# Kernel tuning notes

Hardware: AMD Instinct MI355X
Metric: run time of the kernel (lower is better)

The kernel has to match this reference:

```python
import jax, jax.numpy as jnp
import numpy as np

B, T, N, M = 64, 128, 128, 512


def setup_inputs() -> dict:
    key = jax.random.key(0)
    ks = jax.random.split(key, 9)
    w = 0.02
    return dict(
        X=jax.random.normal(ks[0], (B, T, N), jnp.float32),
        h0=jax.random.normal(ks[1], (B, M), jnp.float32) * 0.05,
        s0=jax.random.normal(ks[2], (B, M), jnp.float32) * 0.05,
        # LSTM cell params (keras gate order: i, f, c, o)
        W_lstm=jax.random.normal(ks[3], (N, 4 * M), jnp.float32) * w,
        U_lstm=jax.random.normal(ks[4], (M, 4 * M), jnp.float32) * w,
        b_lstm=jnp.zeros((4 * M,), jnp.float32),
        # InputAttention params: W_e: Dense(T) on concat([h,c]) (2m -> T),
        # U_e: Dense(T) on X^T (T -> T), v_e: Dense(1) (T -> 1)
        W_e=jax.random.normal(ks[5], (2 * M, T), jnp.float32) * w,
        b_We=jnp.zeros((T,), jnp.float32),
        U_e=jax.random.normal(ks[6], (T, T), jnp.float32) * w,
        b_Ue=jnp.zeros((T,), jnp.float32),
        v_e=jax.random.normal(ks[7], (T, 1), jnp.float32) * w,
        b_ve=jnp.zeros((1,), jnp.float32),
    )


def reference(X, h0, s0, W_lstm, U_lstm, b_lstm, W_e, b_We, U_e, b_Ue, v_e, b_ve):
    # In the original, every loop iteration t runs a single LSTM step on
    # X[:, t, :] starting from the SAME initial_state [h0, s0] (state is not
    # carried across t), so all T steps are independent -> vectorize over T.
    z = jnp.einsum('btn,nk->btk', X, W_lstm) + (h0 @ U_lstm + b_lstm)[:, None, :]
    zi, zf, zc, zo = jnp.split(z, 4, axis=-1)  # keras gate order i,f,c,o
    i = jax.nn.sigmoid(zi)
    f = jax.nn.sigmoid(zf)
    o = jax.nn.sigmoid(zo)
    c = f * s0[:, None, :] + i * jnp.tanh(zc)  # (B, T, m)
    h = o * jnp.tanh(c)                        # (B, T, m)

    # InputAttention for every t at once:
    # e_t = v_e(tanh(W_e([h_t; c_t]) broadcast over n  +  U_e(X^T)))
    hc = jnp.concatenate([h, c], axis=-1)              # (B, T, 2m)
    A = hc @ W_e + b_We                                # (B, T, T)
    U = jnp.einsum('btn,tk->bnk', X, U_e) + b_Ue       # (B, n, T)
    e = jnp.tanh(A[:, :, None, :] + U[:, None, :, :])  # (B, T, n, T)
    scores = jnp.einsum('btnk,k->btn', e, v_e[:, 0]) + b_ve[0]  # (B, T, n)
    alpha = jax.nn.softmax(scores, axis=-1)            # softmax over n
    return X * alpha
```

## Files before the change

kernel.cpp:

```cpp
#include <hip/hip_runtime.h>

typedef __attribute__((ext_vector_type(8))) short bfrag;
typedef __attribute__((ext_vector_type(4))) float f32x4;

#define C_SCALE 2.885390081777926815f

__device__ __forceinline__ float fast_rcp(float x){
#if __has_builtin(__builtin_amdgcn_rcpf)
  return __builtin_amdgcn_rcpf(x);
#else
  return 1.0f/x;
#endif
}
__device__ __forceinline__ float fexp2(float x){
#if __has_builtin(__builtin_amdgcn_exp2f)
  return __builtin_amdgcn_exp2f(x);
#else
  return exp2f(x);
#endif
}
__device__ __forceinline__ float sigm(float x){ return fast_rcp(1.0f + __expf(-x)); }
__device__ __forceinline__ float tanh_f(float x){ return 1.0f - 2.0f*fast_rcp(__expf(2.0f*x) + 1.0f); }
__device__ __forceinline__ unsigned short f2bf(float f){
  unsigned u = __float_as_uint(f);
  return (unsigned short)((u + 0x7fffu + ((u>>16)&1u)) >> 16);
}
__device__ __forceinline__ void gload16(const void* g, void* l){
  __builtin_amdgcn_global_load_lds((const __attribute__((address_space(1))) void*)g,
                                   (__attribute__((address_space(3))) void*)l, 16, 0, 0);
}

__global__ __launch_bounds__(256) void prep(const float* __restrict__ X,
                                            unsigned short* __restrict__ Xbf,
                                            const float* __restrict__ Wl,
                                            unsigned short* __restrict__ Wlt,
                                            const float* __restrict__ We,
                                            unsigned short* __restrict__ Wet,
                                            const float* __restrict__ h0,
                                            const float* __restrict__ Ul,
                                            float* __restrict__ Uhp,
                                            const float* __restrict__ Ue,
                                            const float* __restrict__ bUe,
                                            unsigned short* __restrict__ UTb){
  __shared__ __align__(16) float sh[6600];
  const int tid = threadIdx.x;
  const int bid = blockIdx.x;

  if (bid < 512){
    const int i = (bid*256 + tid)*8;
    float4 a = *(const float4*)&X[i];
    float4 b = *(const float4*)&X[i+4];
    ushort4 lo, hi;
    lo.x=f2bf(a.x); lo.y=f2bf(a.y); lo.z=f2bf(a.z); lo.w=f2bf(a.w);
    hi.x=f2bf(b.x); hi.y=f2bf(b.y); hi.z=f2bf(b.z); hi.w=f2bf(b.w);
    *(ushort4*)&Xbf[i] = lo; *(ushort4*)&Xbf[i+4] = hi;
  } else if (bid < 608){
    const float* in; unsigned short* outp; int K, N, j0, k0, perm;
    if (bid < 576){ int r = bid-512; in = Wl; outp = Wlt; K = 128;  N = 2048; j0 = (r&31)*64; k0 = (r>>5)*64; perm = 0; }
    else          { int r = bid-576; in = We; outp = Wet; K = 1024; N = 128;  j0 = (r&1)*64;  k0 = (r>>1)*64; perm = 1; }
    float (*t)[68] = (float(*)[68])sh;
#pragma unroll
    for (int i=0;i<4;i++){
      int idx = tid + i*256;
      int r = idx>>4, c4 = idx&15;
      int kk = k0 + r;
      int srow = perm ? ((kk&1) ? 512 + (kk>>1) : (kk>>1)) : kk;
      *(float4*)&t[r][c4*4] = *(const float4*)&in[srow*N + j0 + c4*4];
    }
    __syncthreads();
#pragma unroll
    for (int i=0;i<4;i++){
      int idx = tid + i*256;
      int r = idx>>4, c4 = idx&15;
      ushort4 o;
      o.x = f2bf(t[c4*4+0][r]); o.y = f2bf(t[c4*4+1][r]);
      o.z = f2bf(t[c4*4+2][r]); o.w = f2bf(t[c4*4+3][r]);
      *(ushort4*)&outp[(j0+r)*K + k0 + c4*4] = o;
    }
  } else if (bid < 736){
    const int r = bid - 608;
    const int nh = r & 1, b = r >> 1;
    float (*Xs)[68]  = (float(*)[68])sh;
    float (*Us)[132] = (float(*)[132])(sh + 2176);
    const int tc5 = tid & 31, tr8 = tid >> 5;
    f32x4 a4[8];
#pragma unroll
    for (int j=0;j<8;j++) a4[j] = (f32x4){0.f,0.f,0.f,0.f};
    for (int tk=0; tk<4; tk++){
#pragma unroll
      for (int i=0;i<2;i++){
        int idx = tid + i*256;
        int t = idx>>4, nq = idx&15;
        *(float4*)&Xs[t][nq*4] = *(const float4*)&X[(b*128 + tk*32 + t)*128 + nh*64 + nq*4];
      }
#pragma unroll
      for (int i=0;i<4;i++){
        int idx = tid + i*256;
        int t = idx>>5, kq = idx&31;
        *(float4*)&Us[t][kq*4] = *(const float4*)&Ue[(tk*32+t)*128 + kq*4];
      }
      __syncthreads();
#pragma unroll 4
      for (int t=0;t<32;t++){
        f32x4 u4 = *(const f32x4*)&Us[t][tc5*4];
        f32x4 x0 = *(const f32x4*)&Xs[t][tr8*8];
        f32x4 x1 = *(const f32x4*)&Xs[t][tr8*8+4];
        a4[0] += x0.x*u4; a4[1] += x0.y*u4; a4[2] += x0.z*u4; a4[3] += x0.w*u4;
        a4[4] += x1.x*u4; a4[5] += x1.y*u4; a4[6] += x1.z*u4; a4[7] += x1.w*u4;
      }
      __syncthreads();
    }
    const f32x4 bu = *(const f32x4*)&bUe[tc5*4];
    const int ktile = tc5 >> 1, khalf = tc5 & 1;
#pragma unroll
    for (int j=0;j<8;j++){
      const int n = nh*64 + tr8*8 + j;
      f32x4 v = a4[j] + bu;
      ushort4 o;
      o.x = f2bf(fexp2(C_SCALE*v.x)); o.y = f2bf(fexp2(C_SCALE*v.y));
      o.z = f2bf(fexp2(C_SCALE*v.z)); o.w = f2bf(fexp2(C_SCALE*v.w));
      *(ushort4*)&UTb[b*16384 + ktile*1024 + n*8 + khalf*4] = o;
    }
  } else {
    const int r = bid - 736;
    const int jc = r & 15;
    const int bc = (r>>4) >> 2, kc = (r>>4) & 3;
    float (*h0s)[128] = (float(*)[128])sh;
#pragma unroll
    for (int i=0;i<2;i++){
      int idx = tid + i*256;
      int bi = idx>>5, kq = idx&31;
      *(float4*)&h0s[bi][kq*4] = *(const float4*)&h0[(bc*16+bi)*512 + kc*128 + kq*4];
    }
    __syncthreads();
    const int jj = tid & 127, bh = tid >> 7;
    const int j = jc*128 + jj;
    float acc[8];
#pragma unroll
    for (int i=0;i<8;i++) acc[i]=0.f;
    for (int k=0;k<128;k+=4){
      float w0 = Ul[(kc*128+k+0)*2048 + j];
      float w1 = Ul[(kc*128+k+1)*2048 + j];
      float w2 = Ul[(kc*128+k+2)*2048 + j];
      float w3 = Ul[(kc*128+k+3)*2048 + j];
#pragma unroll
      for (int bi=0;bi<8;bi++){
        float4 h4 = *(const float4*)&h0s[bh*8+bi][k];
        acc[bi] += h4.x*w0 + h4.y*w1 + h4.z*w2 + h4.w*w3;
      }
    }
#pragma unroll
    for (int bi=0;bi<8;bi++)
      Uhp[kc*131072 + (bc*16 + bh*8 + bi)*2048 + j] = acc[bi];
  }
}

__global__ __launch_bounds__(256) void k2_k(const unsigned short* __restrict__ Xbf,
                                            const unsigned short* __restrict__ Wlt,
                                            const float* __restrict__ Uhp,
                                            const float* __restrict__ bl,
                                            const float* __restrict__ s0,
                                            unsigned int* __restrict__ hci){
  __shared__ __align__(16) char lds[32768];
  const int tid = threadIdx.x;
  const int mc = blockIdx.x & 15, b = blockIdx.x >> 4;
  const int bt0 = b*128;
  const int lane = tid & 63, wave = tid >> 6;
  const int wr = wave >> 1, wc = wave & 1;

  f32x4 acc[4][4];
#pragma unroll
  for (int mt=0;mt<4;mt++)
#pragma unroll
    for (int nt=0;nt<4;nt++) acc[mt][nt] = (f32x4){0.f,0.f,0.f,0.f};

  for (int kh=0; kh<2; kh++){
#pragma unroll
    for (int i=0;i<4;i++){
      int g = tid + i*256;
      int r = g>>3, G = g&7;
      gload16(Xbf + (bt0+r)*128 + kh*64 + ((G ^ (r&7))<<3), lds + g*16);
    }
#pragma unroll
    for (int i=0;i<4;i++){
      int g = tid + i*256;
      int c = g>>3, G = g&7;
      int q = c>>4;
      int j = (q&3)*512 + mc*32 + ((q>>2)<<4) + (c&15);
      gload16(Wlt + j*128 + kh*64 + ((G ^ (c&7))<<3), lds + 16384 + g*16);
    }
    __syncthreads();
#pragma unroll
    for (int ks2=0; ks2<2; ks2++){
      const int kb = ks2*64 + ((lane>>4)<<4);
      bfrag a[4], bb[4];
#pragma unroll
      for (int mt=0;mt<4;mt++){
        int r = wr*64 + mt*16 + (lane&15);
        a[mt] = *(const bfrag*)&lds[r*128 + (kb ^ ((r&7)<<4))];
      }
#pragma unroll
      for (int nt=0;nt<4;nt++){
        int c = wc*64 + nt*16 + (lane&15);
        bb[nt] = *(const bfrag*)&lds[16384 + c*128 + (kb ^ ((c&7)<<4))];
      }
#pragma unroll
      for (int mt=0;mt<4;mt++)
#pragma unroll
        for (int nt=0;nt<4;nt++)
          acc[mt][nt] = __builtin_amdgcn_mfma_f32_16x16x32_bf16(a[mt], bb[nt], acc[mt][nt], 0, 0, 0);
    }
    __syncthreads();
  }

  const int mloc = mc*32 + wc*16 + (lane&15);
  float uh[4];
#pragma unroll
  for (int g=0;g<4;g++){
    int j = g*512 + mloc;
    uh[g] = bl[j] + Uhp[0*131072 + b*2048 + j] + Uhp[1*131072 + b*2048 + j]
                  + Uhp[2*131072 + b*2048 + j] + Uhp[3*131072 + b*2048 + j];
  }
  const float s0v = s0[b*512 + mloc];
#pragma unroll
  for (int mt=0;mt<4;mt++){
#pragma unroll
    for (int reg=0;reg<4;reg++){
      int row = wr*64 + mt*16 + (lane>>4)*4 + reg;
      float zi = acc[mt][0][reg] + uh[0];
      float zf = acc[mt][1][reg] + uh[1];
      float zc = acc[mt][2][reg] + uh[2];
      float zo = acc[mt][3][reg] + uh[3];
      float fi = sigm(zi), ff = sigm(zf), fo = sigm(zo);
      float cv = ff*s0v + fi*tanh_f(zc);
      float hv = fo*tanh_f(cv);
      hci[(bt0+row)*512 + mloc] = (unsigned)f2bf(hv) | ((unsigned)f2bf(cv) << 16);
    }
  }
}

__global__ __launch_bounds__(256) void k3_k(const unsigned short* __restrict__ hc,
                                            const unsigned short* __restrict__ Wet,
                                            const float* __restrict__ bWe,
                                            float* __restrict__ eA){
  __shared__ __align__(16) char lds[24576];
  const int nc = blockIdx.x & 1, rc = blockIdx.x >> 1;
  const int bt0 = rc*32;
  const int tid = threadIdx.x;
  const int lane = tid & 63, wave = tid >> 6;
  const int wr = wave >> 1, wc = wave & 1;

  f32x4 acc[2];
  acc[0] = (f32x4){0.f,0.f,0.f,0.f};
  acc[1] = (f32x4){0.f,0.f,0.f,0.f};

  for (int ks=0; ks<8; ks++){
    const int k0 = ks*128;
#pragma unroll
    for (int i=0;i<2;i++){
      int g = tid + i*256;
      int r = g>>4, G = g&15;
      gload16(hc + (bt0+r)*1024 + k0 + ((G ^ (r&7))<<3), lds + g*16);
    }
#pragma unroll
    for (int i=0;i<4;i++){
      int g = tid + i*256;
      int r = g>>4, G = g&15;
      gload16(Wet + (nc*64 + r)*1024 + k0 + ((G ^ (r&7))<<3), lds + 8192 + g*16);
    }
    __syncthreads();
#pragma unroll
    for (int kk=0;kk<4;kk++){
      const int kb = kk*64 + ((lane>>4)<<4);
      int r = wr*16 + (lane&15);
      bfrag a = *(const bfrag*)&lds[r*256 + (kb ^ ((r&7)<<4))];
      bfrag bb0, bb1;
      {
        int nn = wc*32 + 0*16 + (lane&15);
        bb0 = *(const bfrag*)&lds[8192 + nn*256 + (kb ^ ((nn&7)<<4))];
        nn = wc*32 + 1*16 + (lane&15);
        bb1 = *(const bfrag*)&lds[8192 + nn*256 + (kb ^ ((nn&7)<<4))];
      }
      acc[0] = __builtin_amdgcn_mfma_f32_16x16x32_bf16(a, bb0, acc[0], 0, 0, 0);
      acc[1] = __builtin_amdgcn_mfma_f32_16x16x32_bf16(a, bb1, acc[1], 0, 0, 0);
    }
    __syncthreads();
  }
#pragma unroll
  for (int reg=0; reg<4; reg++){
    int row = bt0 + wr*16 + (lane>>4)*4 + reg;
#pragma unroll
    for (int nt=0;nt<2;nt++){
      int col = nc*64 + wc*32 + nt*16 + (lane&15);
      eA[row*128 + col] = fexp2(C_SCALE*(acc[nt][reg] + bWe[col]));
    }
  }
}

__global__ __launch_bounds__(256) void k5_k(const float* __restrict__ X,
                                            const unsigned short* __restrict__ UTb,
                                            const float* __restrict__ eA,
                                            const float* __restrict__ ve,
                                            float* __restrict__ out){
  __shared__ __align__(16) float As[8*128];
  __shared__ __align__(16) float vs[128];
  __shared__ float redm[4][4], reds[4][4];
  const int tid = threadIdx.x;
  const int tch = blockIdx.x;
  const int b   = blockIdx.y;
  const int tpair = tid>>7, n = tid&127, wid = tid>>6;

  {
    const float* asrc = eA + (b*128 + tch*8)*128;
    gload16(asrc + tid*4, (char*)As + tid*16);
    if (tid < 128) vs[tid] = ve[tid];
  }
  __syncthreads();

  f32x4 sc[4];
#pragma unroll
  for (int tt=0;tt<4;tt++) sc[tt] = (f32x4){0.f,0.f,0.f,0.f};

  const unsigned short* urow = UTb + b*16384 + n*8;
#pragma unroll 4
  for (int k8=0; k8<16; k8++){
    uint4 u = *(const uint4*)(urow + k8*1024);
    f32x4 ua, ub;
    ua.x = __uint_as_float(u.x<<16); ua.y = __uint_as_float(u.x & 0xffff0000u);
    ua.z = __uint_as_float(u.y<<16); ua.w = __uint_as_float(u.y & 0xffff0000u);
    ub.x = __uint_as_float(u.z<<16); ub.y = __uint_as_float(u.z & 0xffff0000u);
    ub.z = __uint_as_float(u.w<<16); ub.w = __uint_as_float(u.w & 0xffff0000u);
    const f32x4 va = *(const f32x4*)&vs[k8*8];
    const f32x4 vb = *(const f32x4*)&vs[k8*8+4];
#pragma unroll
    for (int tt=0; tt<4; tt++){
      const float* Ar = &As[(tt*2+tpair)*128 + k8*8];
      f32x4 ea = *(const f32x4*)Ar;
      f32x4 eb = *(const f32x4*)(Ar+4);
      f32x4 ra, rb;
      ra.x = fast_rcp(ea.x*ua.x + 1.f); ra.y = fast_rcp(ea.y*ua.y + 1.f);
      ra.z = fast_rcp(ea.z*ua.z + 1.f); ra.w = fast_rcp(ea.w*ua.w + 1.f);
      rb.x = fast_rcp(eb.x*ub.x + 1.f); rb.y = fast_rcp(eb.y*ub.y + 1.f);
      rb.z = fast_rcp(eb.z*ub.z + 1.f); rb.w = fast_rcp(eb.w*ub.w + 1.f);
      sc[tt] += va*ra;
      sc[tt] += vb*rb;
    }
  }

  float sv[4];
#pragma unroll
  for (int tt=0;tt<4;tt++){
    float s = -2.f*((sc[tt].x + sc[tt].y) + (sc[tt].z + sc[tt].w));
    sv[tt] = s;
    float m = s;
#pragma unroll
    for (int off=32; off>0; off>>=1) m = fmaxf(m, __shfl_xor(m, off));
    if ((tid&63)==0) redm[wid][tt] = m;
  }
  __syncthreads();
  float evv[4];
#pragma unroll
  for (int tt=0;tt<4;tt++){
    const float M = fmaxf(redm[tpair*2][tt], redm[tpair*2+1][tt]);
    float e = __expf(sv[tt] - M);
    evv[tt] = e;
    float s = e;
#pragma unroll
    for (int off=32; off>0; off>>=1) s += __shfl_xor(s, off);
    if ((tid&63)==0) reds[wid][tt] = s;
  }
  __syncthreads();
#pragma unroll
  for (int tt=0;tt<4;tt++){
    const float S = reds[tpair*2][tt] + reds[tpair*2+1][tt];
    const float alpha = evv[tt] * fast_rcp(S);
    const int t = tch*8 + tt*2 + tpair;
    const int g = (b*128 + t)*128 + n;
    out[g] = X[g] * alpha;
  }
}

extern "C" void kernel_launch(void* const* d_in, const int* in_sizes, int n_in,
                              void* d_out, int out_size, void* d_ws, size_t ws_size,
                              hipStream_t stream){
  (void)in_sizes; (void)n_in; (void)out_size; (void)ws_size;
  const float* X   = (const float*)d_in[0];
  const float* h0  = (const float*)d_in[1];
  const float* s0  = (const float*)d_in[2];
  const float* Wl  = (const float*)d_in[3];
  const float* Ul  = (const float*)d_in[4];
  const float* bl  = (const float*)d_in[5];
  const float* We  = (const float*)d_in[6];
  const float* bWe = (const float*)d_in[7];
  const float* Ue  = (const float*)d_in[8];
  const float* bUe = (const float*)d_in[9];
  const float* ve  = (const float*)d_in[10];
  float* out = (float*)d_out;

  char* ws = (char*)d_ws;
  unsigned short* Wlt = (unsigned short*)(ws + 0);
  unsigned short* Wet = (unsigned short*)(ws + 524288);
  unsigned short* Xbf = (unsigned short*)(ws + 786432);
  unsigned short* UTb = (unsigned short*)(ws + 2883584);
  unsigned short* hc  = (unsigned short*)(ws + 4980736);
  float*          Uhp = (float*)(ws + 21757952);
  float*          eA  = (float*)(ws + 23855104);
  unsigned int*   hci = (unsigned int*)hc;

  prep <<<dim3(992),    256, 0, stream>>>(X, Xbf, Wl, Wlt, We, Wet, h0, Ul, Uhp, Ue, bUe, UTb);
  k2_k <<<dim3(1024),   256, 0, stream>>>(Xbf, Wlt, Uhp, bl, s0, hci);
  k3_k <<<dim3(512),    256, 0, stream>>>(hc, Wet, bWe, eA);
  k5_k <<<dim3(16,64),  256, 0, stream>>>(X, UTb, eA, ve, out);
}
```

Measured before the change: 61.97 us.

## Fuse attention-logit GEMM into softmax kernel, keeping exp(A) tile in LDS

Result: slower. 65.04 us (+5.0%).

```diff
diff --git a/kernel.cpp b/kernel.cpp
--- a/kernel.cpp
+++ b/kernel.cpp
@@ -239,16 +239,25 @@
   }
 }
 
-__global__ __launch_bounds__(256) void k3_k(const unsigned short* __restrict__ hc,
-                                            const unsigned short* __restrict__ Wet,
-                                            const float* __restrict__ bWe,
-                                            float* __restrict__ eA){
-  __shared__ __align__(16) char lds[24576];
-  const int nc = blockIdx.x & 1, rc = blockIdx.x >> 1;
-  const int bt0 = rc*32;
+__global__ __launch_bounds__(256) void k35(const unsigned short* __restrict__ hc,
+                                           const unsigned short* __restrict__ Wet,
+                                           const float* __restrict__ bWe,
+                                           const float* __restrict__ X,
+                                           const unsigned short* __restrict__ UTb,
+                                           const float* __restrict__ ve,
+                                           float* __restrict__ out){
+  __shared__ __align__(16) char ldsA[4096];
+  __shared__ __align__(16) char ldsB[32768];
+  __shared__ __align__(16) float eAs[16][132];
+  __shared__ __align__(16) float vs[128];
+  __shared__ float redm[4][8], reds[4][8];
   const int tid = threadIdx.x;
+  const int tpc = blockIdx.x;
+  const int b   = blockIdx.y;
+  const int t0  = tpc*16;
   const int lane = tid & 63, wave = tid >> 6;
-  const int wr = wave >> 1, wc = wave & 1;
+
+  if (tid < 128) vs[tid] = ve[tid];
 
   f32x4 acc[2];
   acc[0] = (f32x4){0.f,0.f,0.f,0.f};
@@ -256,73 +265,50 @@
 
   for (int ks=0; ks<8; ks++){
     const int k0 = ks*128;
-#pragma unroll
-    for (int i=0;i<2;i++){
+    {
+      int r = tid>>4, G = tid&15;
+      gload16(hc + (b*128 + t0 + r)*1024 + k0 + ((G ^ (r&7))<<3), ldsA + tid*16);
+    }
+#pragma unroll
+    for (int i=0;i<8;i++){
       int g = tid + i*256;
-      int r = g>>4, G = g&15;
-      gload16(hc + (bt0+r)*1024 + k0 + ((G ^ (r&7))<<3), lds + g*16);
-    }
-#pragma unroll
-    for (int i=0;i<4;i++){
-      int g = tid + i*256;
-      int r = g>>4, G = g&15;
-      gload16(Wet + (nc*64 + r)*1024 + k0 + ((G ^ (r&7))<<3), lds + 8192 + g*16);
+      int n = g>>4, G = g&15;
+      gload16(Wet + n*1024 + k0 + ((G ^ (n&7))<<3), ldsB + g*16);
     }
     __syncthreads();
 #pragma unroll
     for (int kk=0;kk<4;kk++){
       const int kb = kk*64 + ((lane>>4)<<4);
-      int r = wr*16 + (lane&15);
-      bfrag a = *(const bfrag*)&lds[r*256 + (kb ^ ((r&7)<<4))];
-      bfrag bb0, bb1;
-      {
-        int nn = wc*32 + 0*16 + (lane&15);
-        bb0 = *(const bfrag*)&lds[8192 + nn*256 + (kb ^ ((nn&7)<<4))];
-        nn = wc*32 + 1*16 + (lane&15);
-        bb1 = *(const bfrag*)&lds[8192 + nn*256 + (kb ^ ((nn&7)<<4))];
-      }
-      acc[0] = __builtin_amdgcn_mfma_f32_16x16x32_bf16(a, bb0, acc[0], 0, 0, 0);
-      acc[1] = __builtin_amdgcn_mfma_f32_16x16x32_bf16(a, bb1, acc[1], 0, 0, 0);
-    }
-    __syncthreads();
-  }
-#pragma unroll
-  for (int reg=0; reg<4; reg++){
-    int row = bt0 + wr*16 + (lane>>4)*4 + reg;
-#pragma unroll
-    for (int nt=0;nt<2;nt++){
-      int col = nc*64 + wc*32 + nt*16 + (lane&15);
-      eA[row*128 + col] = fexp2(C_SCALE*(acc[nt][reg] + bWe[col]));
-    }
-  }
-}
-
-__global__ __launch_bounds__(256) void k5_k(const float* __restrict__ X,
-                                            const unsigned short* __restrict__ UTb,
-                                            const float* __restrict__ eA,
-                                            const float* __restrict__ ve,
-                                            float* __restrict__ out){
-  __shared__ __align__(16) float As[8*128];
-  __shared__ __align__(16) float vs[128];
-  __shared__ float redm[4][4], reds[4][4];
-  const int tid = threadIdx.x;
-  const int tch = blockIdx.x;
-  const int b   = blockIdx.y;
+      const int r = lane & 15;
+      bfrag a = *(const bfrag*)&ldsA[r*256 + (kb ^ ((r&7)<<4))];
+      const int c0 = wave*32 + (lane&15);
+      bfrag b0 = *(const bfrag*)&ldsB[c0*256 + (kb ^ ((c0&7)<<4))];
+      const int c1 = c0 + 16;
+      bfrag b1 = *(const bfrag*)&ldsB[c1*256 + (kb ^ ((c1&7)<<4))];
+      acc[0] = __builtin_amdgcn_mfma_f32_16x16x32_bf16(a, b0, acc[0], 0, 0, 0);
+      acc[1] = __builtin_amdgcn_mfma_f32_16x16x32_bf16(a, b1, acc[1], 0, 0, 0);
+    }
+    __syncthreads();
+  }
+#pragma unroll
+  for (int nt=0;nt<2;nt++){
+    const int col = wave*32 + nt*16 + (lane&15);
+    const float bw = bWe[col];
+#pragma unroll
+    for (int reg=0;reg<4;reg++){
+      const int row = (lane>>4)*4 + reg;
+      eAs[row][col] = fexp2(C_SCALE*(acc[nt][reg] + bw));
+    }
+  }
+  __syncthreads();
+
   const int tpair = tid>>7, n = tid&127, wid = tid>>6;
-
-  {
-    const float* asrc = eA + (b*128 + tch*8)*128;
-    gload16(asrc + tid*4, (char*)As + tid*16);
-    if (tid < 128) vs[tid] = ve[tid];
-  }
-  __syncthreads();
-
-  f32x4 sc[4];
-#pragma unroll
-  for (int tt=0;tt<4;tt++) sc[tt] = (f32x4){0.f,0.f,0.f,0.f};
+  f32x4 sc[8];
+#pragma unroll
+  for (int tt=0;tt<8;tt++) sc[tt] = (f32x4){0.f,0.f,0.f,0.f};
 
   const unsigned short* urow = UTb + b*16384 + n*8;
-#pragma unroll 4
+#pragma unroll 2
   for (int k8=0; k8<16; k8++){
     uint4 u = *(const uint4*)(urow + k8*1024);
     f32x4 ua, ub;
@@ -333,8 +319,8 @@
     const f32x4 va = *(const f32x4*)&vs[k8*8];
     const f32x4 vb = *(const f32x4*)&vs[k8*8+4];
 #pragma unroll
-    for (int tt=0; tt<4; tt++){
-      const float* Ar = &As[(tt*2+tpair)*128 + k8*8];
+    for (int tt=0; tt<8; tt++){
+      const float* Ar = &eAs[tt*2+tpair][k8*8];
       f32x4 ea = *(const f32x4*)Ar;
       f32x4 eb = *(const f32x4*)(Ar+4);
       f32x4 ra, rb;
@@ -347,9 +333,9 @@
     }
   }
 
-  float sv[4];
-#pragma unroll
-  for (int tt=0;tt<4;tt++){
+  float sv[8];
+#pragma unroll
+  for (int tt=0;tt<8;tt++){
     float s = -2.f*((sc[tt].x + sc[tt].y) + (sc[tt].z + sc[tt].w));
     sv[tt] = s;
     float m = s;
@@ -358,9 +344,9 @@
     if ((tid&63)==0) redm[wid][tt] = m;
   }
   __syncthreads();
-  float evv[4];
-#pragma unroll
-  for (int tt=0;tt<4;tt++){
+  float evv[8];
+#pragma unroll
+  for (int tt=0;tt<8;tt++){
     const float M = fmaxf(redm[tpair*2][tt], redm[tpair*2+1][tt]);
     float e = __expf(sv[tt] - M);
     evv[tt] = e;
@@ -371,10 +357,10 @@
   }
   __syncthreads();
 #pragma unroll
-  for (int tt=0;tt<4;tt++){
+  for (int tt=0;tt<8;tt++){
     const float S = reds[tpair*2][tt] + reds[tpair*2+1][tt];
     const float alpha = evv[tt] * fast_rcp(S);
-    const int t = tch*8 + tt*2 + tpair;
+    const int t = t0 + tt*2 + tpair;
     const int g = (b*128 + t)*128 + n;
     out[g] = X[g] * alpha;
   }
@@ -404,11 +390,9 @@
   unsigned short* UTb = (unsigned short*)(ws + 2883584);
   unsigned short* hc  = (unsigned short*)(ws + 4980736);
   float*          Uhp = (float*)(ws + 21757952);
-  float*          eA  = (float*)(ws + 23855104);
   unsigned int*   hci = (unsigned int*)hc;
 
-  prep <<<dim3(992),    256, 0, stream>>>(X, Xbf, Wl, Wlt, We, Wet, h0, Ul, Uhp, Ue, bUe, UTb);
-  k2_k <<<dim3(1024),   256, 0, stream>>>(Xbf, Wlt, Uhp, bl, s0, hci);
-  k3_k <<<dim3(512),    256, 0, stream>>>(hc, Wet, bWe, eA);
-  k5_k <<<dim3(16,64),  256, 0, stream>>>(X, UTb, eA, ve, out);
-}
+  prep <<<dim3(992),   256, 0, stream>>>(X, Xbf, Wl, Wlt, We, Wet, h0, Ul, Uhp, Ue, bUe, UTb);
+  k2_k <<<dim3(1024),  256, 0, stream>>>(Xbf, Wlt, Uhp, bl, s0, hci);
+  k35  <<<dim3(8,64),  256, 0, stream>>>(hc, Wet, bWe, X, UTb, ve, out);
+}
```
